# Kernel optimization log

Hardware: AMD Instinct MI355X
Metric: run time of the kernel (lower is better)

## Reference

```python
import jax, jax.numpy as jnp
import numpy as np

N, C, H, W = 8, 192, 112, 112
TEMPERATURE = 0.1


def setup_inputs() -> dict:
    key = jax.random.key(0)
    k1, k2 = jax.random.split(key)
    features = jax.random.normal(k1, (N, C, H, W), dtype=jnp.float32)
    # Raw per-pixel directions in {-1, 0, 1}; clip the neighbor coordinate into
    # bounds and recompute the direction so EVERY neighbor is valid. The torch
    # module's broadcasting (labels[:, i, j] vs an (N, M) gather) only works when
    # all N neighbors are valid at each pixel, so this matches its assumptions.
    raw = jax.random.randint(k2, (N, 2, H, W), -1, 2)
    ii = jnp.arange(H)[None, :, None]
    jj = jnp.arange(W)[None, None, :]
    d0 = jnp.clip(ii + raw[:, 0], 0, H - 1) - ii
    d1 = jnp.clip(jj + raw[:, 1], 0, W - 1) - jj
    directions = jnp.stack([d0, d1], axis=1).astype(jnp.int32)
    # Single-class labels: the original loss is -inf whenever any mask entry is 0
    # (log of exactly 0), so a finite, comparable baseline needs matching labels.
    labels = jnp.zeros((N, H, W), dtype=jnp.int32)
    return {"features": features, "labels": labels, "directions": directions}


def reference(features, labels, directions):
    # F.normalize(features, dim=1): x / max(||x||_2, eps)
    norm = jnp.linalg.norm(features, axis=1, keepdims=True)
    fn = features / jnp.maximum(norm, 1e-12)

    ii = jnp.arange(H)[None, :, None]
    jj = jnp.arange(W)[None, None, :]
    ni = ii + directions[:, 0]  # (N, H, W), in-bounds by construction
    nj = jj + directions[:, 1]  # (N, H, W)

    # Torch: features[:, :, neighbor_i, neighbor_j] gathers the M(==N) neighbor
    # coordinates across ALL batch elements -> (N, C, N, H, W) = [n, c, m, i, j]
    gathered = fn[:, :, ni, nj]
    # logits[n, m, i, j] = <fn[n, :, i, j], fn[n, :, ni[m,i,j], nj[m,i,j]]> / T
    logits = jnp.einsum('ncij,ncmij->nmij', fn, gathered) / TEMPERATURE

    # mask[n, m, i, j] = (labels[m, i, j] == labels[n, ni[m,i,j], nj[m,i,j]])
    # (torch broadcasts labels[:, i, j] along the first axis of the (N, M) gather)
    labels_g = labels[:, ni, nj]  # (N, N, H, W) = [n, m, i, j]
    mask = (labels[None, :, :, :] == labels_g).astype(fn.dtype)

    exp_l = jnp.exp(logits) * mask
    denom = jnp.sum(exp_l, axis=1, keepdims=True)  # sum over m
    # sum_{i,j} mean_{n,m}(.) / (H*W) == global mean over (n, m, i, j)
    loss = (-jnp.log(exp_l / (denom + 1e-6))).mean()
    return loss
```

## Files before the change

kernel.cpp:

```cpp
#include <hip/hip_runtime.h>
#include <math.h>


namespace {
constexpr int N_ = 8, C_ = 192, H_ = 112, W_ = 112;
constexpr int HW = H_ * W_;
constexpr int TH = 4;
constexpr int TROWS = TH + 2;
constexpr int TWID = W_ + 2;
constexpr int TILE_E = TROWS * TWID;
constexpr int NT = TH * W_;
constexpr int EXTRA = TILE_E - NT;
constexpr int K_ = 4;
constexpr int NCHUNK = C_ / K_;
constexpr float INV_T = 10.0f;
constexpr double TOTAL = (double)N_ * N_ * H_ * W_;
}

__device__ __forceinline__ float sel3(int d, float a, float b, float c) {
    float r = (d < 0) ? a : b;
    return (d > 0) ? c : r;
}

extern "C" __global__ void __launch_bounds__(NT)
dcl_main(const float* __restrict__ feat,
         const int* __restrict__ labels,
         const int* __restrict__ dirs,
         double* __restrict__ acc)
{
    __shared__ float tiles[2][K_][TILE_E];
    __shared__ float ssbuf[TILE_E];
    __shared__ float red[8];

    const int tid = threadIdx.x;
    const int n   = blockIdx.y;
    const int gy0 = blockIdx.x * TH;

    int gofs0, gofs1 = 0;
    {
        int r = tid / TWID, col = tid - r * TWID;
        gofs0 = min(max(gy0 + r - 1, 0), H_ - 1) * W_ + min(max(col - 1, 0), W_ - 1);
        if (tid < EXTRA) {
            int t2 = tid + NT;
            r = t2 / TWID; col = t2 - r * TWID;
            gofs1 = min(max(gy0 + r - 1, 0), H_ - 1) * W_ + min(max(col - 1, 0), W_ - 1);
        }
    }

    const int ty = tid / W_;
    const int tx = tid - ty * W_;
    const int gi = gy0 + ty;
    const int gj = tx;
    const int ci = (ty + 1) * TWID + (tx + 1);

    const float* plane = feat + (size_t)n * C_ * HW;

    float ss0 = 0.0f, ss1 = 0.0f;

    #pragma unroll
    for (int k = 0; k < K_; ++k) {
        float v = plane[(size_t)k * HW + gofs0];
        tiles[0][k][tid] = v; ss0 += v * v;
    }
    if (tid < EXTRA) {
        #pragma unroll
        for (int k = 0; k < K_; ++k) {
            float v = plane[(size_t)k * HW + gofs1];
            tiles[0][k][tid + NT] = v; ss1 += v * v;
        }
    }
    __syncthreads();

    float s00=0.f, s01=0.f, s02=0.f;
    float s10=0.f, s11=0.f, s12=0.f;
    float s20=0.f, s21=0.f, s22=0.f;

    for (int t = 0; t < NCHUNK; ++t) {
        float pv0[K_], pv1[K_];
        const bool more = (t + 1 < NCHUNK);
        if (more) {
            const float* p = plane + (size_t)(t + 1) * K_ * HW;
            #pragma unroll
            for (int k = 0; k < K_; ++k) pv0[k] = p[(size_t)k * HW + gofs0];
            if (tid < EXTRA) {
                #pragma unroll
                for (int k = 0; k < K_; ++k) pv1[k] = p[(size_t)k * HW + gofs1];
            }
        }

        const float* cur = &tiles[t & 1][0][0];
        #pragma unroll
        for (int k = 0; k < K_; ++k) {
            const float* cp = cur + k * TILE_E;
            float fc = cp[ci];
            s00 += fc * cp[ci - TWID - 1];
            s01 += fc * cp[ci - TWID];
            s02 += fc * cp[ci - TWID + 1];
            s10 += fc * cp[ci - 1];
            s11 += fc * fc;
            s12 += fc * cp[ci + 1];
            s20 += fc * cp[ci + TWID - 1];
            s21 += fc * cp[ci + TWID];
            s22 += fc * cp[ci + TWID + 1];
        }

        if (more) {
            float* nxt = &tiles[(t + 1) & 1][0][0];
            #pragma unroll
            for (int k = 0; k < K_; ++k) {
                float v = pv0[k];
                nxt[k * TILE_E + tid] = v; ss0 += v * v;
            }
            if (tid < EXTRA) {
                #pragma unroll
                for (int k = 0; k < K_; ++k) {
                    float v = pv1[k];
                    nxt[k * TILE_E + tid + NT] = v; ss1 += v * v;
                }
            }
        }
        __syncthreads();
    }

    ssbuf[tid] = 1.0f / fmaxf(sqrtf(ss0), 1e-12f);
    if (tid < EXTRA)
        ssbuf[tid + NT] = 1.0f / fmaxf(sqrtf(ss1), 1e-12f);
    __syncthreads();

    const float invc = ssbuf[ci] * INV_T;
    const float l00 = s00 * invc * ssbuf[ci - TWID - 1];
    const float l01 = s01 * invc * ssbuf[ci - TWID];
    const float l02 = s02 * invc * ssbuf[ci - TWID + 1];
    const float l10 = s10 * invc * ssbuf[ci - 1];
    const float l11 = s11 * invc * ssbuf[ci];
    const float l12 = s12 * invc * ssbuf[ci + 1];
    const float l20 = s20 * invc * ssbuf[ci + TWID - 1];
    const float l21 = s21 * invc * ssbuf[ci + TWID];
    const float l22 = s22 * invc * ssbuf[ci + TWID + 1];

    const int pix = gi * W_ + gj;
    float denom = 0.0f;
    float sumlog = 0.0f;
    #pragma unroll
    for (int m = 0; m < N_; ++m) {
        int d0 = dirs[((m * 2 + 0) * H_ + gi) * W_ + gj];
        int d1 = dirs[((m * 2 + 1) * H_ + gi) * W_ + gj];
        float r0 = sel3(d1, l00, l01, l02);
        float r1 = sel3(d1, l10, l11, l12);
        float r2 = sel3(d1, l20, l21, l22);
        float lm = sel3(d0, r0, r1, r2);
        int labm = labels[m * HW + pix];
        int labn = labels[n * HW + (gi + d0) * W_ + (gj + d1)];
        bool mask = (labm == labn);
        float e = mask ? __expf(lm) : 0.0f;
        denom += e;
        sumlog += mask ? lm : -INFINITY;
    }
    float logd = __logf(denom + 1e-6f);
    float lp = 8.0f * logd - sumlog;

    #pragma unroll
    for (int off = 32; off > 0; off >>= 1)
        lp += __shfl_down(lp, off, 64);
    const int wave = tid >> 6, lane = tid & 63;
    if (lane == 0) red[wave] = lp;
    __syncthreads();
    if (tid == 0) {
        float s = 0.0f;
        #pragma unroll
        for (int w = 0; w < NT / 64; ++w) s += red[w];
        atomicAdd(acc, (double)s);
    }
}

extern "C" __global__ void dcl_final(const double* __restrict__ acc,
                                     float* __restrict__ out)
{
    out[0] = (float)(acc[0] / TOTAL);
}

extern "C" void kernel_launch(void* const* d_in, const int* in_sizes, int n_in,
                              void* d_out, int out_size, void* d_ws, size_t ws_size,
                              hipStream_t stream) {
    const float* feat   = (const float*)d_in[0];
    const int*   labels = (const int*)d_in[1];
    const int*   dirs   = (const int*)d_in[2];
    double* acc = (double*)d_ws;
    float*  out = (float*)d_out;

    hipMemsetAsync(acc, 0, sizeof(double), stream);
    dim3 grid(H_ / TH, N_);
    dcl_main<<<grid, NT, 0, stream>>>(feat, labels, dirs, acc);
    dcl_final<<<1, 1, 0, stream>>>(acc, out);
}
```

Before: 144.3 us.

## Split channel reduction across blocks with partial sums and separate loss kernel

Splits the 192-channel dot-product reduction into four slices handled by separate blocks, writing nine neighbor partial sums per pixel to workspace. Separate kernels then combine the partials into inverse norms and compute the loss. The aim is to fill the GPU with about four times as many blocks than the original 224. In exchange it adds extra global traffic for the partials and two more launches, and it falls back to the monolithic kernel if the workspace is too small.

```diff
diff --git a/kernel.cpp b/kernel.cpp
--- a/kernel.cpp
+++ b/kernel.cpp
@@ -5,16 +5,23 @@
 namespace {
 constexpr int N_ = 8, C_ = 192, H_ = 112, W_ = 112;
 constexpr int HW = H_ * W_;
+constexpr int NPIX = N_ * HW;
 constexpr int TH = 4;
 constexpr int TROWS = TH + 2;
 constexpr int TWID = W_ + 2;
 constexpr int TILE_E = TROWS * TWID;
 constexpr int NT = TH * W_;
 constexpr int EXTRA = TILE_E - NT;
-constexpr int K_ = 4;
-constexpr int NCHUNK = C_ / K_;
+constexpr int CSPLIT = 4;
+constexpr int CPB = C_ / CSPLIT;
+constexpr int KCH = 4;
+constexpr int NCHUNK = CPB / KCH;
 constexpr float INV_T = 10.0f;
 constexpr double TOTAL = (double)N_ * N_ * H_ * W_;
+constexpr int NT2 = 256;
+constexpr int NBLK2 = NPIX / NT2;
+constexpr size_t PART_FLOATS = (size_t)CSPLIT * 9 * NPIX;
+constexpr size_t WS_NEEDED = (PART_FLOATS + NPIX) * sizeof(float) + sizeof(double);
 }
 
 __device__ __forceinline__ float sel3(int d, float a, float b, float c) {
@@ -23,18 +30,14 @@
 }
 
 extern "C" __global__ void __launch_bounds__(NT)
-dcl_main(const float* __restrict__ feat,
-         const int* __restrict__ labels,
-         const int* __restrict__ dirs,
-         double* __restrict__ acc)
-{
-    __shared__ float tiles[2][K_][TILE_E];
-    __shared__ float ssbuf[TILE_E];
-    __shared__ float red[8];
-
-    const int tid = threadIdx.x;
-    const int n   = blockIdx.y;
-    const int gy0 = blockIdx.x * TH;
+dcl_part(const float* __restrict__ feat, float* __restrict__ part)
+{
+    __shared__ float2 tiles[2][2][TILE_E];
+
+    const int tid   = threadIdx.x;
+    const int gy0   = blockIdx.x * TH;
+    const int n     = blockIdx.y;
+    const int slice = blockIdx.z;
 
     int gofs0, gofs1 = 0;
     {
@@ -46,137 +49,283 @@
             gofs1 = min(max(gy0 + r - 1, 0), H_ - 1) * W_ + min(max(col - 1, 0), W_ - 1);
         }
     }
-
-    const int ty = tid / W_;
-    const int tx = tid - ty * W_;
-    const int gi = gy0 + ty;
-    const int gj = tx;
+    const int ty = tid / W_, tx = tid - ty * W_;
     const int ci = (ty + 1) * TWID + (tx + 1);
-
+    const float* __restrict__ plane =
+        feat + ((size_t)n * C_ + (size_t)slice * CPB) * HW;
+
+    float s[9];
+    #pragma unroll
+    for (int d = 0; d < 9; ++d) s[d] = 0.0f;
+
+    {
+        float v0 = plane[gofs0], v1 = plane[HW + gofs0];
+        float v2 = plane[2 * HW + gofs0], v3 = plane[3 * HW + gofs0];
+        tiles[0][0][tid] = make_float2(v0, v1);
+        tiles[0][1][tid] = make_float2(v2, v3);
+        if (tid < EXTRA) {
+            float u0 = plane[gofs1], u1 = plane[HW + gofs1];
+            float u2 = plane[2 * HW + gofs1], u3 = plane[3 * HW + gofs1];
+            tiles[0][0][tid + NT] = make_float2(u0, u1);
+            tiles[0][1][tid + NT] = make_float2(u2, u3);
+        }
+    }
+    __syncthreads();
+
+    for (int t = 0; t < NCHUNK; ++t) {
+        float pv[KCH], qv[KCH];
+        const bool more = (t + 1 < NCHUNK);
+        if (more) {
+            const float* p = plane + (size_t)(t + 1) * KCH * HW;
+            #pragma unroll
+            for (int k = 0; k < KCH; ++k) pv[k] = p[(size_t)k * HW + gofs0];
+            if (tid < EXTRA) {
+                #pragma unroll
+                for (int k = 0; k < KCH; ++k) qv[k] = p[(size_t)k * HW + gofs1];
+            }
+        }
+
+        #pragma unroll
+        for (int g = 0; g < 2; ++g) {
+            const float2* __restrict__ cp = tiles[t & 1][g];
+            float2 fc  = cp[ci];
+            float2 n00 = cp[ci - TWID - 1];
+            float2 n01 = cp[ci - TWID];
+            float2 n02 = cp[ci - TWID + 1];
+            float2 n10 = cp[ci - 1];
+            float2 n12 = cp[ci + 1];
+            float2 n20 = cp[ci + TWID - 1];
+            float2 n21 = cp[ci + TWID];
+            float2 n22 = cp[ci + TWID + 1];
+            s[0] = fmaf(fc.x, n00.x, s[0]); s[0] = fmaf(fc.y, n00.y, s[0]);
+            s[1] = fmaf(fc.x, n01.x, s[1]); s[1] = fmaf(fc.y, n01.y, s[1]);
+            s[2] = fmaf(fc.x, n02.x, s[2]); s[2] = fmaf(fc.y, n02.y, s[2]);
+            s[3] = fmaf(fc.x, n10.x, s[3]); s[3] = fmaf(fc.y, n10.y, s[3]);
+            s[4] = fmaf(fc.x, fc.x,  s[4]); s[4] = fmaf(fc.y, fc.y,  s[4]);
+            s[5] = fmaf(fc.x, n12.x, s[5]); s[5] = fmaf(fc.y, n12.y, s[5]);
+            s[6] = fmaf(fc.x, n20.x, s[6]); s[6] = fmaf(fc.y, n20.y, s[6]);
+            s[7] = fmaf(fc.x, n21.x, s[7]); s[7] = fmaf(fc.y, n21.y, s[7]);
+            s[8] = fmaf(fc.x, n22.x, s[8]); s[8] = fmaf(fc.y, n22.y, s[8]);
+        }
+
+        if (more) {
+            float2* nxt0 = tiles[(t + 1) & 1][0];
+            float2* nxt1 = tiles[(t + 1) & 1][1];
+            nxt0[tid] = make_float2(pv[0], pv[1]);
+            nxt1[tid] = make_float2(pv[2], pv[3]);
+            if (tid < EXTRA) {
+                nxt0[tid + NT] = make_float2(qv[0], qv[1]);
+                nxt1[tid + NT] = make_float2(qv[2], qv[3]);
+            }
+        }
+        __syncthreads();
+    }
+
+    const int gpix = n * HW + (gy0 + ty) * W_ + tx;
+    const size_t po = (size_t)slice * 9 * NPIX;
+    #pragma unroll
+    for (int d = 0; d < 9; ++d)
+        part[po + (size_t)d * NPIX + gpix] = s[d];
+}
+
+extern "C" __global__ void __launch_bounds__(NT2)
+dcl_norm(const float* __restrict__ part, float* __restrict__ inv)
+{
+    const int g = blockIdx.x * NT2 + threadIdx.x;
+    float ss = 0.0f;
+    #pragma unroll
+    for (int sl = 0; sl < CSPLIT; ++sl)
+        ss += part[((size_t)sl * 9 + 4) * NPIX + g];
+    inv[g] = 1.0f / fmaxf(sqrtf(ss), 1e-12f);
+}
+
+extern "C" __global__ void __launch_bounds__(NT2)
+dcl_loss(const float* __restrict__ part, const float* __restrict__ inv,
+         const int* __restrict__ labels, const int* __restrict__ dirs,
+         double* __restrict__ acc)
+{
+    const int g   = blockIdx.x * NT2 + threadIdx.x;
+    const int n   = g / HW, pix = g - n * HW;
+    const int gi  = pix / W_, gj = pix - gi * W_;
+
+    float s[9];
+    #pragma unroll
+    for (int d = 0; d < 9; ++d) {
+        float v = part[(size_t)d * NPIX + g];
+        #pragma unroll
+        for (int sl = 1; sl < CSPLIT; ++sl)
+            v += part[((size_t)sl * 9 + d) * NPIX + g];
+        s[d] = v;
+    }
+
+    const float invc = inv[g] * INV_T;
+    const int r0 = n * HW + max(gi - 1, 0) * W_;
+    const int r1 = n * HW + gi * W_;
+    const int r2 = n * HW + min(gi + 1, H_ - 1) * W_;
+    const int c0 = max(gj - 1, 0), c1 = gj, c2 = min(gj + 1, W_ - 1);
+
+    const float l00 = s[0] * invc * inv[r0 + c0];
+    const float l01 = s[1] * invc * inv[r0 + c1];
+    const float l02 = s[2] * invc * inv[r0 + c2];
+    const float l10 = s[3] * invc * inv[r1 + c0];
+    const float l11 = s[4] * invc * inv[r1 + c1];
+    const float l12 = s[5] * invc * inv[r1 + c2];
+    const float l20 = s[6] * invc * inv[r2 + c0];
+    const float l21 = s[7] * invc * inv[r2 + c1];
+    const float l22 = s[8] * invc * inv[r2 + c2];
+
+    float denom = 0.f, sumlog = 0.f;
+    #pragma unroll
+    for (int m = 0; m < N_; ++m) {
+        int d0 = dirs[((m * 2 + 0) * H_ + gi) * W_ + gj];
+        int d1 = dirs[((m * 2 + 1) * H_ + gi) * W_ + gj];
+        float q0 = sel3(d1, l00, l01, l02);
+        float q1 = sel3(d1, l10, l11, l12);
+        float q2 = sel3(d1, l20, l21, l22);
+        float lm = sel3(d0, q0, q1, q2);
+        int labm = labels[m * HW + pix];
+        int labn = labels[n * HW + (gi + d0) * W_ + (gj + d1)];
+        bool msk = (labm == labn);
+        float e = msk ? __expf(lm) : 0.f;
+        denom += e;
+        sumlog += msk ? lm : -INFINITY;
+    }
+    float lp = 8.0f * __logf(denom + 1e-6f) - sumlog;
+
+    #pragma unroll
+    for (int off = 32; off > 0; off >>= 1) lp += __shfl_down(lp, off, 64);
+    __shared__ float red[NT2 / 64];
+    const int lane = threadIdx.x & 63, wv = threadIdx.x >> 6;
+    if (lane == 0) red[wv] = lp;
+    __syncthreads();
+    if (threadIdx.x == 0) {
+        float t = red[0] + red[1] + red[2] + red[3];
+        atomicAdd(acc, (double)t);
+    }
+}
+
+extern "C" __global__ void dcl_final(const double* __restrict__ acc,
+                                     float* __restrict__ out)
+{
+    out[0] = (float)(acc[0] / TOTAL);
+}
+
+extern "C" __global__ void __launch_bounds__(NT)
+dcl_mono(const float* __restrict__ feat,
+         const int* __restrict__ labels,
+         const int* __restrict__ dirs,
+         double* __restrict__ acc)
+{
+    __shared__ float tiles[2][KCH][TILE_E];
+    __shared__ float ssbuf[TILE_E];
+    __shared__ float red[8];
+
+    const int tid = threadIdx.x;
+    const int n   = blockIdx.y;
+    const int gy0 = blockIdx.x * TH;
+
+    int gofs0, gofs1 = 0;
+    {
+        int r = tid / TWID, col = tid - r * TWID;
+        gofs0 = min(max(gy0 + r - 1, 0), H_ - 1) * W_ + min(max(col - 1, 0), W_ - 1);
+        if (tid < EXTRA) {
+            int t2 = tid + NT;
+            r = t2 / TWID; col = t2 - r * TWID;
+            gofs1 = min(max(gy0 + r - 1, 0), H_ - 1) * W_ + min(max(col - 1, 0), W_ - 1);
+        }
+    }
+    const int ty = tid / W_, tx = tid - ty * W_;
+    const int gi = gy0 + ty, gj = tx;
+    const int ci = (ty + 1) * TWID + (tx + 1);
     const float* plane = feat + (size_t)n * C_ * HW;
-
-    float ss0 = 0.0f, ss1 = 0.0f;
-
-    #pragma unroll
-    for (int k = 0; k < K_; ++k) {
+    float ss0 = 0.f, ss1 = 0.f;
+
+    #pragma unroll
+    for (int k = 0; k < KCH; ++k) {
         float v = plane[(size_t)k * HW + gofs0];
         tiles[0][k][tid] = v; ss0 += v * v;
     }
     if (tid < EXTRA) {
         #pragma unroll
-        for (int k = 0; k < K_; ++k) {
+        for (int k = 0; k < KCH; ++k) {
             float v = plane[(size_t)k * HW + gofs1];
             tiles[0][k][tid + NT] = v; ss1 += v * v;
         }
     }
     __syncthreads();
 
-    float s00=0.f, s01=0.f, s02=0.f;
-    float s10=0.f, s11=0.f, s12=0.f;
-    float s20=0.f, s21=0.f, s22=0.f;
-
-    for (int t = 0; t < NCHUNK; ++t) {
-        float pv0[K_], pv1[K_];
-        const bool more = (t + 1 < NCHUNK);
+    float s00=0.f,s01=0.f,s02=0.f,s10=0.f,s11=0.f,s12=0.f,s20=0.f,s21=0.f,s22=0.f;
+    for (int t = 0; t < C_ / KCH; ++t) {
+        float pv0[KCH], pv1[KCH];
+        const bool more = (t + 1 < C_ / KCH);
         if (more) {
-            const float* p = plane + (size_t)(t + 1) * K_ * HW;
+            const float* p = plane + (size_t)(t + 1) * KCH * HW;
             #pragma unroll
-            for (int k = 0; k < K_; ++k) pv0[k] = p[(size_t)k * HW + gofs0];
+            for (int k = 0; k < KCH; ++k) pv0[k] = p[(size_t)k * HW + gofs0];
             if (tid < EXTRA) {
                 #pragma unroll
-                for (int k = 0; k < K_; ++k) pv1[k] = p[(size_t)k * HW + gofs1];
+                for (int k = 0; k < KCH; ++k) pv1[k] = p[(size_t)k * HW + gofs1];
             }
         }
-
         const float* cur = &tiles[t & 1][0][0];
         #pragma unroll
-        for (int k = 0; k < K_; ++k) {
+        for (int k = 0; k < KCH; ++k) {
             const float* cp = cur + k * TILE_E;
             float fc = cp[ci];
-            s00 += fc * cp[ci - TWID - 1];
-            s01 += fc * cp[ci - TWID];
-            s02 += fc * cp[ci - TWID + 1];
-            s10 += fc * cp[ci - 1];
-            s11 += fc * fc;
-            s12 += fc * cp[ci + 1];
-            s20 += fc * cp[ci + TWID - 1];
-            s21 += fc * cp[ci + TWID];
-            s22 += fc * cp[ci + TWID + 1];
-        }
-
+            s00 += fc * cp[ci - TWID - 1]; s01 += fc * cp[ci - TWID]; s02 += fc * cp[ci - TWID + 1];
+            s10 += fc * cp[ci - 1];        s11 += fc * fc;            s12 += fc * cp[ci + 1];
+            s20 += fc * cp[ci + TWID - 1]; s21 += fc * cp[ci + TWID]; s22 += fc * cp[ci + TWID + 1];
+        }
         if (more) {
             float* nxt = &tiles[(t + 1) & 1][0][0];
             #pragma unroll
-            for (int k = 0; k < K_; ++k) {
-                float v = pv0[k];
-                nxt[k * TILE_E + tid] = v; ss0 += v * v;
-            }
+            for (int k = 0; k < KCH; ++k) { float v = pv0[k]; nxt[k*TILE_E+tid]=v; ss0+=v*v; }
             if (tid < EXTRA) {
                 #pragma unroll
-                for (int k = 0; k < K_; ++k) {
-                    float v = pv1[k];
-                    nxt[k * TILE_E + tid + NT] = v; ss1 += v * v;
-                }
+                for (int k = 0; k < KCH; ++k) { float v = pv1[k]; nxt[k*TILE_E+tid+NT]=v; ss1+=v*v; }
             }
         }
         __syncthreads();
     }
 
     ssbuf[tid] = 1.0f / fmaxf(sqrtf(ss0), 1e-12f);
-    if (tid < EXTRA)
-        ssbuf[tid + NT] = 1.0f / fmaxf(sqrtf(ss1), 1e-12f);
+    if (tid < EXTRA) ssbuf[tid + NT] = 1.0f / fmaxf(sqrtf(ss1), 1e-12f);
     __syncthreads();
 
     const float invc = ssbuf[ci] * INV_T;
-    const float l00 = s00 * invc * ssbuf[ci - TWID - 1];
-    const float l01 = s01 * invc * ssbuf[ci - TWID];
-    const float l02 = s02 * invc * ssbuf[ci - TWID + 1];
-    const float l10 = s10 * invc * ssbuf[ci - 1];
-    const float l11 = s11 * invc * ssbuf[ci];
-    const float l12 = s12 * invc * ssbuf[ci + 1];
-    const float l20 = s20 * invc * ssbuf[ci + TWID - 1];
-    const float l21 = s21 * invc * ssbuf[ci + TWID];
-    const float l22 = s22 * invc * ssbuf[ci + TWID + 1];
+    const float l00 = s00*invc*ssbuf[ci-TWID-1], l01 = s01*invc*ssbuf[ci-TWID], l02 = s02*invc*ssbuf[ci-TWID+1];
+    const float l10 = s10*invc*ssbuf[ci-1],      l11 = s11*invc*ssbuf[ci],      l12 = s12*invc*ssbuf[ci+1];
+    const float l20 = s20*invc*ssbuf[ci+TWID-1], l21 = s21*invc*ssbuf[ci+TWID], l22 = s22*invc*ssbuf[ci+TWID+1];
 
     const int pix = gi * W_ + gj;
-    float denom = 0.0f;
-    float sumlog = 0.0f;
+    float denom = 0.f, sumlog = 0.f;
     #pragma unroll
     for (int m = 0; m < N_; ++m) {
         int d0 = dirs[((m * 2 + 0) * H_ + gi) * W_ + gj];
         int d1 = dirs[((m * 2 + 1) * H_ + gi) * W_ + gj];
-        float r0 = sel3(d1, l00, l01, l02);
-        float r1 = sel3(d1, l10, l11, l12);
-        float r2 = sel3(d1, l20, l21, l22);
-        float lm = sel3(d0, r0, r1, r2);
+        float q0 = sel3(d1, l00, l01, l02);
+        float q1 = sel3(d1, l10, l11, l12);
+        float q2 = sel3(d1, l20, l21, l22);
+        float lm = sel3(d0, q0, q1, q2);
         int labm = labels[m * HW + pix];
         int labn = labels[n * HW + (gi + d0) * W_ + (gj + d1)];
-        bool mask = (labm == labn);
-        float e = mask ? __expf(lm) : 0.0f;
-        denom += e;
-        sumlog += mask ? lm : -INFINITY;
-    }
-    float logd = __logf(denom + 1e-6f);
-    float lp = 8.0f * logd - sumlog;
-
-    #pragma unroll
-    for (int off = 32; off > 0; off >>= 1)
-        lp += __shfl_down(lp, off, 64);
+        bool msk = (labm == labn);
+        float e = msk ? __expf(lm) : 0.f;
+        denom += e; sumlog += msk ? lm : -INFINITY;
+    }
+    float lp = 8.0f * __logf(denom + 1e-6f) - sumlog;
+
+    #pragma unroll
+    for (int off = 32; off > 0; off >>= 1) lp += __shfl_down(lp, off, 64);
     const int wave = tid >> 6, lane = tid & 63;
     if (lane == 0) red[wave] = lp;
     __syncthreads();
     if (tid == 0) {
-        float s = 0.0f;
-        #pragma unroll
-        for (int w = 0; w < NT / 64; ++w) s += red[w];
-        atomicAdd(acc, (double)s);
-    }
-}
-
-extern "C" __global__ void dcl_final(const double* __restrict__ acc,
-                                     float* __restrict__ out)
-{
-    out[0] = (float)(acc[0] / TOTAL);
+        float t = 0.f;
+        #pragma unroll
+        for (int w = 0; w < NT / 64; ++w) t += red[w];
+        atomicAdd(acc, (double)t);
+    }
 }
 
 extern "C" void kernel_launch(void* const* d_in, const int* in_sizes, int n_in,
@@ -185,11 +334,21 @@
     const float* feat   = (const float*)d_in[0];
     const int*   labels = (const int*)d_in[1];
     const int*   dirs   = (const int*)d_in[2];
-    double* acc = (double*)d_ws;
-    float*  out = (float*)d_out;
-
-    hipMemsetAsync(acc, 0, sizeof(double), stream);
-    dim3 grid(H_ / TH, N_);
-    dcl_main<<<grid, NT, 0, stream>>>(feat, labels, dirs, acc);
-    dcl_final<<<1, 1, 0, stream>>>(acc, out);
-}
+    float* out = (float*)d_out;
+
+    if (ws_size >= WS_NEEDED) {
+        float*  part = (float*)d_ws;
+        float*  inv  = part + PART_FLOATS;
+        double* acc  = (double*)(inv + NPIX);
+        hipMemsetAsync(acc, 0, sizeof(double), stream);
+        dcl_part<<<dim3(H_ / TH, N_, CSPLIT), NT, 0, stream>>>(feat, part);
+        dcl_norm<<<NBLK2, NT2, 0, stream>>>(part, inv);
+        dcl_loss<<<NBLK2, NT2, 0, stream>>>(part, inv, labels, dirs, acc);
+        dcl_final<<<1, 1, 0, stream>>>(acc, out);
+    } else {
+        double* acc = (double*)d_ws;
+        hipMemsetAsync(acc, 0, sizeof(double), stream);
+        dcl_mono<<<dim3(H_ / TH, N_), NT, 0, stream>>>(feat, labels, dirs, acc);
+        dcl_final<<<1, 1, 0, stream>>>(acc, out);
+    }
+}
```

Result: slower. 259.2 us (+79.6%).

## Halve row tile to double block count and pack LDS channels as float2

Applied to the files above, without the earlier changes.

Rows per block drop from 4 to 2, giving a fixed 256-thread block in which 224 threads own pixels and the rest only help load the halo tile. This doubles the grid from 224 to 448 blocks, so more of the GPU's compute units have work and latency is better hidden, and launch bounds request 2 blocks per unit. The shared-memory tile now stores channel pairs as float2, so each stencil neighbour takes one wider LDS read for two channels, and the barrier after the last chunk is skipped. In exchange, halo rows are a larger share of each tile, which raises redundant global reads of the features.

```diff
diff --git a/kernel.cpp b/kernel.cpp
--- a/kernel.cpp
+++ b/kernel.cpp
@@ -5,14 +5,15 @@
 namespace {
 constexpr int N_ = 8, C_ = 192, H_ = 112, W_ = 112;
 constexpr int HW = H_ * W_;
-constexpr int TH = 4;
+constexpr int TH = 2;
 constexpr int TROWS = TH + 2;
 constexpr int TWID = W_ + 2;
 constexpr int TILE_E = TROWS * TWID;
-constexpr int NT = TH * W_;
+constexpr int NT = 256;
+constexpr int NPX = TH * W_;
 constexpr int EXTRA = TILE_E - NT;
-constexpr int K_ = 4;
-constexpr int NCHUNK = C_ / K_;
+constexpr int KCH = 4;
+constexpr int NCHUNK = C_ / KCH;
 constexpr float INV_T = 10.0f;
 constexpr double TOTAL = (double)N_ * N_ * H_ * W_;
 }
@@ -22,15 +23,15 @@
     return (d > 0) ? c : r;
 }
 
-extern "C" __global__ void __launch_bounds__(NT)
+extern "C" __global__ void __launch_bounds__(NT, 2)
 dcl_main(const float* __restrict__ feat,
          const int* __restrict__ labels,
          const int* __restrict__ dirs,
          double* __restrict__ acc)
 {
-    __shared__ float tiles[2][K_][TILE_E];
+    __shared__ float2 tiles[2][2][TILE_E];
     __shared__ float ssbuf[TILE_E];
-    __shared__ float red[8];
+    __shared__ float red[NT / 64];
 
     const int tid = threadIdx.x;
     const int n   = blockIdx.y;
@@ -47,129 +48,137 @@
         }
     }
 
+    const bool is_px = (tid < NPX);
     const int ty = tid / W_;
     const int tx = tid - ty * W_;
     const int gi = gy0 + ty;
     const int gj = tx;
     const int ci = (ty + 1) * TWID + (tx + 1);
 
-    const float* plane = feat + (size_t)n * C_ * HW;
+    const float* __restrict__ plane = feat + (size_t)n * C_ * HW;
 
     float ss0 = 0.0f, ss1 = 0.0f;
 
+    {
+        float v0 = plane[gofs0], v1 = plane[HW + gofs0];
+        float v2 = plane[2 * HW + gofs0], v3 = plane[3 * HW + gofs0];
+        ss0 += v0 * v0 + v1 * v1 + v2 * v2 + v3 * v3;
+        tiles[0][0][tid] = make_float2(v0, v1);
+        tiles[0][1][tid] = make_float2(v2, v3);
+        if (tid < EXTRA) {
+            float u0 = plane[gofs1], u1 = plane[HW + gofs1];
+            float u2 = plane[2 * HW + gofs1], u3 = plane[3 * HW + gofs1];
+            ss1 += u0 * u0 + u1 * u1 + u2 * u2 + u3 * u3;
+            tiles[0][0][tid + NT] = make_float2(u0, u1);
+            tiles[0][1][tid + NT] = make_float2(u2, u3);
+        }
+    }
+    __syncthreads();
+
+    float s[9];
     #pragma unroll
-    for (int k = 0; k < K_; ++k) {
-        float v = plane[(size_t)k * HW + gofs0];
-        tiles[0][k][tid] = v; ss0 += v * v;
-    }
-    if (tid < EXTRA) {
-        #pragma unroll
-        for (int k = 0; k < K_; ++k) {
-            float v = plane[(size_t)k * HW + gofs1];
-            tiles[0][k][tid + NT] = v; ss1 += v * v;
-        }
-    }
-    __syncthreads();
-
-    float s00=0.f, s01=0.f, s02=0.f;
-    float s10=0.f, s11=0.f, s12=0.f;
-    float s20=0.f, s21=0.f, s22=0.f;
+    for (int d = 0; d < 9; ++d) s[d] = 0.0f;
 
     for (int t = 0; t < NCHUNK; ++t) {
-        float pv0[K_], pv1[K_];
+        float pv0[KCH], pv1[KCH];
         const bool more = (t + 1 < NCHUNK);
         if (more) {
-            const float* p = plane + (size_t)(t + 1) * K_ * HW;
+            const float* p = plane + (size_t)(t + 1) * KCH * HW;
             #pragma unroll
-            for (int k = 0; k < K_; ++k) pv0[k] = p[(size_t)k * HW + gofs0];
+            for (int k = 0; k < KCH; ++k) pv0[k] = p[(size_t)k * HW + gofs0];
             if (tid < EXTRA) {
                 #pragma unroll
-                for (int k = 0; k < K_; ++k) pv1[k] = p[(size_t)k * HW + gofs1];
+                for (int k = 0; k < KCH; ++k) pv1[k] = p[(size_t)k * HW + gofs1];
             }
         }
 
-        const float* cur = &tiles[t & 1][0][0];
-        #pragma unroll
-        for (int k = 0; k < K_; ++k) {
-            const float* cp = cur + k * TILE_E;
-            float fc = cp[ci];
-            s00 += fc * cp[ci - TWID - 1];
-            s01 += fc * cp[ci - TWID];
-            s02 += fc * cp[ci - TWID + 1];
-            s10 += fc * cp[ci - 1];
-            s11 += fc * fc;
-            s12 += fc * cp[ci + 1];
-            s20 += fc * cp[ci + TWID - 1];
-            s21 += fc * cp[ci + TWID];
-            s22 += fc * cp[ci + TWID + 1];
+        if (is_px) {
+            #pragma unroll
+            for (int g = 0; g < 2; ++g) {
+                const float2* __restrict__ cp = tiles[t & 1][g];
+                float2 fc  = cp[ci];
+                float2 n00 = cp[ci - TWID - 1];
+                float2 n01 = cp[ci - TWID];
+                float2 n02 = cp[ci - TWID + 1];
+                float2 n10 = cp[ci - 1];
+                float2 n12 = cp[ci + 1];
+                float2 n20 = cp[ci + TWID - 1];
+                float2 n21 = cp[ci + TWID];
+                float2 n22 = cp[ci + TWID + 1];
+                s[0] = fmaf(fc.x, n00.x, s[0]); s[0] = fmaf(fc.y, n00.y, s[0]);
+                s[1] = fmaf(fc.x, n01.x, s[1]); s[1] = fmaf(fc.y, n01.y, s[1]);
+                s[2] = fmaf(fc.x, n02.x, s[2]); s[2] = fmaf(fc.y, n02.y, s[2]);
+                s[3] = fmaf(fc.x, n10.x, s[3]); s[3] = fmaf(fc.y, n10.y, s[3]);
+                s[4] = fmaf(fc.x, fc.x,  s[4]); s[4] = fmaf(fc.y, fc.y,  s[4]);
+                s[5] = fmaf(fc.x, n12.x, s[5]); s[5] = fmaf(fc.y, n12.y, s[5]);
+                s[6] = fmaf(fc.x, n20.x, s[6]); s[6] = fmaf(fc.y, n20.y, s[6]);
+                s[7] = fmaf(fc.x, n21.x, s[7]); s[7] = fmaf(fc.y, n21.y, s[7]);
+                s[8] = fmaf(fc.x, n22.x, s[8]); s[8] = fmaf(fc.y, n22.y, s[8]);
+            }
         }
 
         if (more) {
-            float* nxt = &tiles[(t + 1) & 1][0][0];
-            #pragma unroll
-            for (int k = 0; k < K_; ++k) {
-                float v = pv0[k];
-                nxt[k * TILE_E + tid] = v; ss0 += v * v;
+            float2* nxt0 = tiles[(t + 1) & 1][0];
+            float2* nxt1 = tiles[(t + 1) & 1][1];
+            ss0 += pv0[0]*pv0[0] + pv0[1]*pv0[1] + pv0[2]*pv0[2] + pv0[3]*pv0[3];
+            nxt0[tid] = make_float2(pv0[0], pv0[1]);
+            nxt1[tid] = make_float2(pv0[2], pv0[3]);
+            if (tid < EXTRA) {
+                ss1 += pv1[0]*pv1[0] + pv1[1]*pv1[1] + pv1[2]*pv1[2] + pv1[3]*pv1[3];
+                nxt0[tid + NT] = make_float2(pv1[0], pv1[1]);
+                nxt1[tid + NT] = make_float2(pv1[2], pv1[3]);
             }
-            if (tid < EXTRA) {
-                #pragma unroll
-                for (int k = 0; k < K_; ++k) {
-                    float v = pv1[k];
-                    nxt[k * TILE_E + tid + NT] = v; ss1 += v * v;
-                }
-            }
-        }
-        __syncthreads();
-    }
-
+            __syncthreads();
+        }
+    }
+
+    __syncthreads();
     ssbuf[tid] = 1.0f / fmaxf(sqrtf(ss0), 1e-12f);
     if (tid < EXTRA)
         ssbuf[tid + NT] = 1.0f / fmaxf(sqrtf(ss1), 1e-12f);
     __syncthreads();
 
-    const float invc = ssbuf[ci] * INV_T;
-    const float l00 = s00 * invc * ssbuf[ci - TWID - 1];
-    const float l01 = s01 * invc * ssbuf[ci - TWID];
-    const float l02 = s02 * invc * ssbuf[ci - TWID + 1];
-    const float l10 = s10 * invc * ssbuf[ci - 1];
-    const float l11 = s11 * invc * ssbuf[ci];
-    const float l12 = s12 * invc * ssbuf[ci + 1];
-    const float l20 = s20 * invc * ssbuf[ci + TWID - 1];
-    const float l21 = s21 * invc * ssbuf[ci + TWID];
-    const float l22 = s22 * invc * ssbuf[ci + TWID + 1];
-
-    const int pix = gi * W_ + gj;
-    float denom = 0.0f;
-    float sumlog = 0.0f;
+    float lp = 0.0f;
+    if (is_px) {
+        const float invc = ssbuf[ci] * INV_T;
+        const float l00 = s[0] * invc * ssbuf[ci - TWID - 1];
+        const float l01 = s[1] * invc * ssbuf[ci - TWID];
+        const float l02 = s[2] * invc * ssbuf[ci - TWID + 1];
+        const float l10 = s[3] * invc * ssbuf[ci - 1];
+        const float l11 = s[4] * invc * ssbuf[ci];
+        const float l12 = s[5] * invc * ssbuf[ci + 1];
+        const float l20 = s[6] * invc * ssbuf[ci + TWID - 1];
+        const float l21 = s[7] * invc * ssbuf[ci + TWID];
+        const float l22 = s[8] * invc * ssbuf[ci + TWID + 1];
+
+        const int pix = gi * W_ + gj;
+        float denom = 0.f, sumlog = 0.f;
+        #pragma unroll
+        for (int m = 0; m < N_; ++m) {
+            int d0 = dirs[((m * 2 + 0) * H_ + gi) * W_ + gj];
+            int d1 = dirs[((m * 2 + 1) * H_ + gi) * W_ + gj];
+            float q0 = sel3(d1, l00, l01, l02);
+            float q1 = sel3(d1, l10, l11, l12);
+            float q2 = sel3(d1, l20, l21, l22);
+            float lm = sel3(d0, q0, q1, q2);
+            int labm = labels[m * HW + pix];
+            int labn = labels[n * HW + (gi + d0) * W_ + (gj + d1)];
+            bool msk = (labm == labn);
+            float e = msk ? __expf(lm) : 0.f;
+            denom += e;
+            sumlog += msk ? lm : -INFINITY;
+        }
+        lp = 8.0f * __logf(denom + 1e-6f) - sumlog;
+    }
+
     #pragma unroll
-    for (int m = 0; m < N_; ++m) {
-        int d0 = dirs[((m * 2 + 0) * H_ + gi) * W_ + gj];
-        int d1 = dirs[((m * 2 + 1) * H_ + gi) * W_ + gj];
-        float r0 = sel3(d1, l00, l01, l02);
-        float r1 = sel3(d1, l10, l11, l12);
-        float r2 = sel3(d1, l20, l21, l22);
-        float lm = sel3(d0, r0, r1, r2);
-        int labm = labels[m * HW + pix];
-        int labn = labels[n * HW + (gi + d0) * W_ + (gj + d1)];
-        bool mask = (labm == labn);
-        float e = mask ? __expf(lm) : 0.0f;
-        denom += e;
-        sumlog += mask ? lm : -INFINITY;
-    }
-    float logd = __logf(denom + 1e-6f);
-    float lp = 8.0f * logd - sumlog;
-
-    #pragma unroll
-    for (int off = 32; off > 0; off >>= 1)
-        lp += __shfl_down(lp, off, 64);
+    for (int off = 32; off > 0; off >>= 1) lp += __shfl_down(lp, off, 64);
     const int wave = tid >> 6, lane = tid & 63;
     if (lane == 0) red[wave] = lp;
     __syncthreads();
     if (tid == 0) {
-        float s = 0.0f;
-        #pragma unroll
-        for (int w = 0; w < NT / 64; ++w) s += red[w];
-        atomicAdd(acc, (double)s);
+        float t = red[0] + red[1] + red[2] + red[3];
+        atomicAdd(acc, (double)t);
     }
 }
 
```

Result: faster. 136.7 us (-5.3%).
